# Kernel optimization log

Measured on AMD Instinct MI355X. Metric: run time of the kernel, lower is better.

Reference implementation:

```python
import jax, jax.numpy as jnp
import numpy as np

D_MODEL = 1024
N_HEADS = 16
HEAD_DIM = D_MODEL // N_HEADS
D_FF = 4096
B, S = 2, 2048


def layer_norm(x, gamma, beta, eps=1e-5):
    mu = jnp.mean(x, axis=-1, keepdims=True)
    var = jnp.mean(jnp.square(x - mu), axis=-1, keepdims=True)
    return (x - mu) * jax.lax.rsqrt(var + eps) * gamma + beta


def setup_inputs() -> dict:
    key = jax.random.key(0)
    ks = jax.random.split(key, 8)
    s = 0.02
    return {
        "x": jax.random.normal(ks[0], (B, S, D_MODEL), dtype=jnp.float32),
        "qkv_w": jax.random.normal(ks[1], (D_MODEL, 3 * D_MODEL), dtype=jnp.float32) * s,
        "qkv_b": jnp.zeros((3 * D_MODEL,), jnp.float32),
        "out_w": jax.random.normal(ks[2], (D_MODEL, D_MODEL), dtype=jnp.float32) * s,
        "out_b": jnp.zeros((D_MODEL,), jnp.float32),
        "attn_ln_g": jnp.ones((D_MODEL,), jnp.float32),
        "attn_ln_b": jnp.zeros((D_MODEL,), jnp.float32),
        "norm1_g": jnp.ones((D_MODEL,), jnp.float32),
        "norm1_b": jnp.zeros((D_MODEL,), jnp.float32),
        "ff_ln_g": jnp.ones((D_MODEL,), jnp.float32),
        "ff_ln_b": jnp.zeros((D_MODEL,), jnp.float32),
        "w1": jax.random.normal(ks[3], (D_MODEL, D_FF), dtype=jnp.float32) * s,
        "b1": jnp.zeros((D_FF,), jnp.float32),
        "w2": jax.random.normal(ks[4], (D_FF, D_MODEL), dtype=jnp.float32) * s,
        "b2": jnp.zeros((D_MODEL,), jnp.float32),
        "norm2_g": jnp.ones((D_MODEL,), jnp.float32),
        "norm2_b": jnp.zeros((D_MODEL,), jnp.float32),
    }


def reference(x, qkv_w, qkv_b, out_w, out_b, attn_ln_g, attn_ln_b,
              norm1_g, norm1_b, ff_ln_g, ff_ln_b, w1, b1, w2, b2,
              norm2_g, norm2_b):
    # --- MultiHeadAttention (pre-LN inside the attn block) ---
    h = layer_norm(x, attn_ln_g, attn_ln_b)
    qkv = h @ qkv_w + qkv_b                       # [B,S,3D]
    qkv = qkv.reshape(B, S, 3, N_HEADS, HEAD_DIM)
    q = jnp.transpose(qkv[:, :, 0], (0, 2, 1, 3))  # [B,H,S,hd]
    k = jnp.transpose(qkv[:, :, 1], (0, 2, 1, 3))
    v = jnp.transpose(qkv[:, :, 2], (0, 2, 1, 3))
    scale = HEAD_DIM ** -0.5
    scores = jnp.einsum("bhqd,bhkd->bhqk", q, k) * scale  # [B,H,S,S]
    attn = jax.nn.softmax(scores, axis=-1)
    ctx = jnp.einsum("bhqk,bhkd->bhqd", attn, v)
    ctx = jnp.transpose(ctx, (0, 2, 1, 3)).reshape(B, S, D_MODEL)
    attn_out = ctx @ out_w + out_b

    # residual + post-LN
    x = layer_norm(x + attn_out, norm1_g, norm1_b)

    # --- FeedForward (pre-LN inside the FF block, GELU) ---
    h = layer_norm(x, ff_ln_g, ff_ln_b)
    ff = jax.nn.gelu(h @ w1 + b1, approximate=False) @ w2 + b2

    # residual + post-LN
    return layer_norm(x + ff, norm2_g, norm2_b)
```

## Files before the change

kernel.cpp:

```cpp
#include <hip/hip_runtime.h>
#include <hip/hip_bf16.h>

typedef __attribute__((ext_vector_type(4))) float f32x4;
typedef __attribute__((ext_vector_type(16))) float f32x16;
typedef __attribute__((ext_vector_type(8))) short s16x8;
typedef __attribute__((ext_vector_type(4))) short s16x4;

#define DM 1024
#define NH 16
#define NB 2
#define NS 2048
#define NTOK (NB*NS)

__device__ __forceinline__ float b2f(short u){
  union { unsigned int i; float f; } c; c.i = ((unsigned int)(unsigned short)u) << 16; return c.f;
}
__device__ __forceinline__ short f2b(float f){
  __hip_bfloat16 h = __float2bfloat16(f);
  return __builtin_bit_cast(short, h);
}
__device__ __forceinline__ unsigned pk2(float lo, float hi){
  unsigned ul = __builtin_bit_cast(unsigned, lo);
  unsigned uh = __builtin_bit_cast(unsigned, hi);
  return (uh & 0xFFFF0000u) | (ul >> 16);
}
__device__ __forceinline__ float ex2(float x){
  float r;
  asm("v_exp_f32 %0, %1" : "=v"(r) : "v"(x));
  return r;
}
__device__ __forceinline__ void gload16(const void* g, void* l){
  __builtin_amdgcn_global_load_lds((const __attribute__((address_space(1))) void*)g,
                                   (__attribute__((address_space(3))) void*)l, 16, 0, 0);
}
__device__ __forceinline__ s16x4 tr16(const void* p){
  s16x4 r;
  asm volatile("ds_read_b64_tr_b16 %0, %1"
               : "=v"(r)
               : "v"((const __attribute__((address_space(3))) short*)p)
               : "memory");
  return r;
}

#define BARX { __builtin_amdgcn_sched_barrier(0); __builtin_amdgcn_s_barrier(); __builtin_amdgcn_sched_barrier(0); }
#define LGK  { asm volatile("s_waitcnt lgkmcnt(0)" ::: "memory"); __builtin_amdgcn_sched_barrier(0); }

template<int MIH>
__device__ __forceinline__ void rdA(s16x8 (&Af)[4][2], const short* Ab, int foff){
  #pragma unroll
  for (int m=0;m<4;m++)
    #pragma unroll
    for (int ks=0;ks<2;ks++)
      Af[m][ks] = *(const s16x8*)(Ab + (MIH*4+m)*1024 + ks*512 + foff);
}
template<int NIH>
__device__ __forceinline__ void rdB(s16x8 (&Bf)[4][2], const short* Bb, int foff){
  #pragma unroll
  for (int n=0;n<2;n++)
    #pragma unroll
    for (int ks=0;ks<2;ks++)
      Bf[NIH*2+n][ks] = *(const s16x8*)(Bb + (NIH*2+n)*1024 + ks*512 + foff);
}
template<int MIH,int NIH>
__device__ __forceinline__ void mmQ(f32x4 (&acc)[8][4], s16x8 (&Af)[4][2], s16x8 (&Bf)[4][2]){
  __builtin_amdgcn_s_setprio(1);
  #pragma unroll
  for (int m=0;m<4;m++)
    #pragma unroll
    for (int n=0;n<2;n++)
      #pragma unroll
      for (int ks=0;ks<2;ks++)
        acc[MIH*4+m][NIH*2+n] = __builtin_amdgcn_mfma_f32_16x16x32_bf16(
            Af[m][ks], Bf[NIH*2+n][ks], acc[MIH*4+m][NIH*2+n], 0,0,0);
  __builtin_amdgcn_s_setprio(0);
}

template<int GELU, int SPLITS>
__global__ __launch_bounds__(512,2) void gemm8p(
    const short* __restrict__ A, const short* __restrict__ Bt,
    const float* __restrict__ bias,
    short* __restrict__ C0, short* __restrict__ C1,
    short* __restrict__ C2, short* __restrict__ C3,
    int M, int N, int Ktot)
{
  __shared__ short Al[2*16384];
  __shared__ short Bl[2*16384];
  int tid = threadIdx.x, wid = tid>>6, lane = tid&63;
  int la = lane&15, lb = lane>>4;
  int z = blockIdx.z;
  const int Ksp = Ktot / SPLITS;
  short* C = (SPLITS==1) ? C0 : (z==0?C0 : z==1?C1 : z==2?C2 : C3);
  const short* Az  = A  + z*Ksp;
  const short* Btz = Bt + z*Ksp;
  int nbn = N>>8;
  int nwg = (M>>8)*nbn;
  int bid = (int)blockIdx.x;
  int sid = (bid&7)*(nwg>>3) + (bid>>3);
  int bm = sid / nbn, bn = sid % nbn;
  int wm2 = wid>>2, wn4 = wid&3;
  int bhalf = wn4>>1, bq4 = (wn4&1)*4;

  const short* aA0 = Az  + (size_t)(bm*256)*Ktot;
  const short* aA1 = Az  + (size_t)(bm*256+128)*Ktot;
  const short* bB0 = Btz + (size_t)(bn*256)*Ktot;
  const short* bB1 = Btz + (size_t)(bn*256+128)*Ktot;

  auto stG = [&](short* dstHalf, const short* srcRow0, int kt){
    #pragma unroll
    for (int c=0;c<2;c++){
      int s = c*8 + wid;
      int row = ((s>>1)<<4) + (lane>>2);
      int kk  = kt + ((s&1)<<5) + (((lane&3)<<3) ^ ((lane&32)>>1));
      gload16(srcRow0 + (size_t)row*Ktot + kk, dstHalf + s*512);
    }
  };

  int NJ = Ksp>>7;
  stG(&Al[0], aA0, 0);      stG(&Al[8192], aA1, 0);
  stG(&Bl[0], bB0, 0);      stG(&Bl[8192], bB1, 0);
  stG(&Bl[16384], bB0, 64); stG(&Bl[16384+8192], bB1, 64);
  asm volatile("s_waitcnt vmcnt(4)" ::: "memory");
  BARX;

  f32x4 acc[8][4] = {};
  s16x8 Af[4][2], Bf[4][2];
  int foff = la*32 + ((lb*8) ^ ((la&8)<<1));

  const short* Ab0c = &Al[wm2*8192];
  const short* Ab1c = &Al[16384 + wm2*8192];
  const short* Bb0c = &Bl[bhalf*8192 + bq4*1024];
  const short* Bb1c = &Bl[16384 + bhalf*8192 + bq4*1024];

  for (int j=0;j<NJ;j++){
    bool more = (j+1 < NJ);
    int ktA  = (2*j+1)*64;
    int ktN0 = (2*j+2)*64, ktN1 = (2*j+3)*64;
    rdA<0>(Af, Ab0c, foff); rdB<0>(Bf, Bb0c, foff);
    stG(&Al[16384], aA0, ktA);
    BARX; LGK; mmQ<0,0>(acc,Af,Bf); BARX;
    rdB<1>(Bf, Bb0c, foff);
    stG(&Al[16384+8192], aA1, ktA);
    BARX; LGK; mmQ<0,1>(acc,Af,Bf); BARX;
    rdA<1>(Af, Ab0c, foff);
    if (more) stG(&Bl[0], bB0, ktN0);
    BARX; LGK; mmQ<1,1>(acc,Af,Bf); BARX;
    if (more){ stG(&Bl[8192], bB1, ktN0);
               asm volatile("s_waitcnt vmcnt(4)" ::: "memory"); }
    else     { asm volatile("s_waitcnt vmcnt(0)" ::: "memory"); }
    BARX; mmQ<1,0>(acc,Af,Bf); BARX;
    rdA<0>(Af, Ab1c, foff); rdB<0>(Bf, Bb1c, foff);
    if (more) stG(&Al[0], aA0, ktN0);
    BARX; LGK; mmQ<0,0>(acc,Af,Bf); BARX;
    rdB<1>(Bf, Bb1c, foff);
    if (more) stG(&Al[8192], aA1, ktN0);
    BARX; LGK; mmQ<0,1>(acc,Af,Bf); BARX;
    rdA<1>(Af, Ab1c, foff);
    if (more) stG(&Bl[16384], bB0, ktN1);
    BARX; LGK; mmQ<1,1>(acc,Af,Bf); BARX;
    if (more){ stG(&Bl[16384+8192], bB1, ktN1);
               asm volatile("s_waitcnt vmcnt(4)" ::: "memory"); }
    else     { asm volatile("s_waitcnt vmcnt(0)" ::: "memory"); }
    BARX; mmQ<1,0>(acc,Af,Bf); BARX;
  }

  #pragma unroll
  for (int ni=0;ni<4;ni++){
    int col = bn*256 + wn4*64 + ni*16 + la;
    float bv = (SPLITS==1 || z==0) ? bias[col] : 0.0f;
    #pragma unroll
    for (int mi=0;mi<8;mi++){
      int row0 = bm*256 + wm2*128 + mi*16 + lb*4;
      #pragma unroll
      for (int j=0;j<4;j++){
        float v = acc[mi][ni][j] + bv;
        if (GELU) v = 0.5f*v*(1.0f + erff(v*0.70710678118f));
        C[(size_t)(row0+j)*N + col] = f2b(v);
      }
    }
  }
}

__global__ __launch_bounds__(512,1) void attn_fwd(const short* __restrict__ qkv, short* __restrict__ ctx)
{
  __shared__ short KlS[2*4096];
  __shared__ short VlS[2*4096];
  __shared__ float stats[8*32];
  char* Kl = (char*)KlS; char* Vl = (char*)VlS;
  int tid=threadIdx.x, w=tid>>6, lane=tid&63;
  int q5=lane&31, hi=lane>>5, la=lane&15, lb0=(lane>>4)&1;
  int qt=blockIdx.x, bh=blockIdx.y;
  int b=bh>>4, h=bh&15;
  int q0w = qt*256 + w*32;

  const float QSC = 0.125f * 1.44269504f;
  const short* qp = qkv + (size_t)(b*NS+q0w+q5)*3072 + h*64 + hi*8;
  s16x8 qf[4];
  #pragma unroll
  for (int ds=0; ds<4; ds++){
    s16x8 v = *(const s16x8*)(qp + ds*16);
    #pragma unroll
    for (int j=0;j<8;j++) v[j] = f2b(b2f(v[j])*QSC);
    qf[ds]=v;
  }

  int krow = 8*w + (lane>>3);
  int kcolS = (((lane&7) ^ ((lane>>3)&7)) << 3);
  const short* Ksrc = qkv + (size_t)(b*NS+krow)*3072 + h*64 + 1024 + kcolS;
  int vk = 16*(w&3) + 8*hi + 4*lb0 + ((lane>>1)&3);
  int vd = 32*(w>>2) + 16*((lane>>3)&1) + 8*(lane&1);
  const short* Vsrc = qkv + (size_t)(b*NS+vk)*3072 + h*64 + 2048 + vd;

  int sw = (q5&7)<<4;
  int baseK = q5*128 + ((hi<<4) ^ (sw&16)) + (sw&96);
  int baseV = hi*512 + lb0*128 + la*8;

  f32x16 cacc0={}, cacc1={};
  float mrow=-1e30f, lrow=0.f;
  const size_t tstep = (size_t)64*3072;

  gload16(Ksrc, Kl + w*1024);
  gload16(Vsrc, Vl + w*1024);
  __syncthreads();
  int cur=0;

  for (int t=0;t<NS/64;t++){
    if (t+1 < NS/64){
      gload16(Ksrc + (size_t)(t+1)*tstep, Kl + (cur^1)*8192 + w*1024);
      gload16(Vsrc + (size_t)(t+1)*tstep, Vl + (cur^1)*8192 + w*1024);
    }
    const char* Kb = Kl + cur*8192;
    f32x16 s0={}, s1={};
    #pragma unroll
    for (int ds=0; ds<4; ds++){
      s16x8 k0 = *(const s16x8*)(Kb + (baseK ^ (ds<<5)));
      s16x8 k1 = *(const s16x8*)(Kb + 4096 + (baseK ^ (ds<<5)));
      s0 = __builtin_amdgcn_mfma_f32_32x32x16_bf16(k0, qf[ds], s0, 0,0,0);
      s1 = __builtin_amdgcn_mfma_f32_32x32x16_bf16(k1, qf[ds], s1, 0,0,0);
    }
    float pmax = s0[0];
    #pragma unroll
    for (int r=1;r<16;r++) pmax = fmaxf(pmax, s0[r]);
    #pragma unroll
    for (int r=0;r<16;r++) pmax = fmaxf(pmax, s1[r]);
    pmax = fmaxf(pmax, __shfl_xor(pmax, 32, 64));
    if (__any(pmax > mrow + 8.f)){
      float mnew = fmaxf(mrow, pmax);
      float corr = ex2(mrow - mnew);
      if (!hi) stats[w*32+q5] = corr;
      LGK;
      lrow *= corr; mrow = mnew;
      #pragma unroll
      for (int r=0;r<16;r++){
        float c = stats[w*32 + ((r&3)+8*(r>>2)+4*hi)];
        cacc0[r]*=c; cacc1[r]*=c;
      }
    }
    float rs = 0.f;
    #pragma unroll
    for (int r=0;r<16;r++){ float p=ex2(s0[r]-mrow); s0[r]=p; rs+=p; }
    #pragma unroll
    for (int r=0;r<16;r++){ float p=ex2(s1[r]-mrow); s1[r]=p; rs+=p; }
    rs += __shfl_xor(rs, 32, 64);
    lrow += rs;
    unsigned int D0[4][2], D1[4][2], R0[4][2], R1[4][2];
    #pragma unroll
    for (int bb=0;bb<4;bb++)
      #pragma unroll
      for (int hh=0;hh<2;hh++){
        D0[bb][hh] = pk2(s0[4*bb+2*hh], s0[4*bb+2*hh+1]);
        D1[bb][hh] = pk2(s1[4*bb+2*hh], s1[4*bb+2*hh+1]);
      }
    #pragma unroll
    for (int bb=0;bb<4;bb++)
      #pragma unroll
      for (int hh=0;hh<2;hh++){
        R0[bb][hh] = (unsigned int)__shfl_xor((int)D0[bb][hh], 32, 64);
        R1[bb][hh] = (unsigned int)__shfl_xor((int)D1[bb][hh], 32, 64);
      }
    union PA { unsigned int u[4]; s16x8 v; } pa[4];
    #pragma unroll
    for (int e=0;e<2;e++)
      #pragma unroll
      for (int hh=0;hh<2;hh++){
        pa[e].u[hh]     = hi ? R0[2*e+1][hh] : D0[2*e][hh];
        pa[e].u[2+hh]   = hi ? D0[2*e+1][hh] : R0[2*e][hh];
        pa[2+e].u[hh]   = hi ? R1[2*e+1][hh] : D1[2*e][hh];
        pa[2+e].u[2+hh] = hi ? D1[2*e+1][hh] : R1[2*e][hh];
      }
    const char* Vb = Vl + cur*8192;
    #pragma unroll
    for (int ks=0;ks<4;ks++){
      s16x4 t00 = tr16(Vb + ks*1024 +        0 + baseV);
      s16x4 t01 = tr16(Vb + ks*1024 +      256 + baseV);
      s16x4 t10 = tr16(Vb + ks*1024 + 4096     + baseV);
      s16x4 t11 = tr16(Vb + ks*1024 + 4096+256 + baseV);
      LGK;
      union { s16x4 hh[2]; s16x8 v; } u0, u1;
      u0.hh[0]=t00; u0.hh[1]=t01;
      u1.hh[0]=t10; u1.hh[1]=t11;
      cacc0 = __builtin_amdgcn_mfma_f32_32x32x16_bf16(pa[ks].v, u0.v, cacc0, 0,0,0);
      cacc1 = __builtin_amdgcn_mfma_f32_32x32x16_bf16(pa[ks].v, u1.v, cacc1, 0,0,0);
    }
    __syncthreads();
    cur ^= 1;
  }
  if (!hi) stats[w*32+q5] = 1.0f/lrow;
  LGK;
  #pragma unroll
  for (int r=0;r<16;r++){
    int q = (r&3)+8*(r>>2)+4*hi;
    float linv = stats[w*32+q];
    size_t row = (size_t)(b*NS + q0w + q)*DM + h*64;
    ctx[row + q5]      = f2b(cacc0[r]*linv);
    ctx[row + 32 + q5] = f2b(cacc1[r]*linv);
  }
}

__device__ __forceinline__ void wred2(float& s, float& ss){
  #pragma unroll
  for (int m=1;m<64;m<<=1){ s += __shfl_xor(s,m,64); ss += __shfl_xor(ss,m,64); }
}

__global__ __launch_bounds__(256) void ln_in(const float* __restrict__ x,
    const float* __restrict__ g, const float* __restrict__ be, short* __restrict__ out)
{
  int row=blockIdx.x, tid=threadIdx.x;
  __shared__ float r1[4], r2[4];
  float4 v = ((const float4*)(x + (size_t)row*DM))[tid];
  float s=v.x+v.y+v.z+v.w, ss=v.x*v.x+v.y*v.y+v.z*v.z+v.w*v.w;
  wred2(s,ss);
  if ((tid&63)==0){ r1[tid>>6]=s; r2[tid>>6]=ss; }
  __syncthreads();
  s=r1[0]+r1[1]+r1[2]+r1[3]; ss=r2[0]+r2[1]+r2[2]+r2[3];
  float mu=s*(1.f/DM);
  float rstd=rsqrtf(ss*(1.f/DM)-mu*mu+1e-5f);
  float4 gv=((const float4*)g)[tid], bv=((const float4*)be)[tid];
  s16x4 o;
  o[0]=f2b((v.x-mu)*rstd*gv.x+bv.x);
  o[1]=f2b((v.y-mu)*rstd*gv.y+bv.y);
  o[2]=f2b((v.z-mu)*rstd*gv.z+bv.z);
  o[3]=f2b((v.w-mu)*rstd*gv.w+bv.w);
  *(s16x4*)(out + (size_t)row*DM + tid*4) = o;
}

__global__ __launch_bounds__(256) void ln_chain(const float* __restrict__ x,
    const short* __restrict__ p0, const short* __restrict__ p1,
    const short* __restrict__ p2, const short* __restrict__ p3,
    const float* __restrict__ g1, const float* __restrict__ be1,
    const float* __restrict__ g2, const float* __restrict__ be2,
    float* __restrict__ x1, short* __restrict__ h2)
{
  int row=blockIdx.x, tid=threadIdx.x;
  __shared__ float r1[4], r2[4], r3[4], r4[4];
  size_t off = (size_t)row*DM + tid*4;
  float4 xv = ((const float4*)(x + (size_t)row*DM))[tid];
  s16x4 a0=*(const s16x4*)(p0+off), a1=*(const s16x4*)(p1+off);
  s16x4 a2=*(const s16x4*)(p2+off), a3=*(const s16x4*)(p3+off);
  float4 y;
  y.x = xv.x + b2f(a0[0])+b2f(a1[0])+b2f(a2[0])+b2f(a3[0]);
  y.y = xv.y + b2f(a0[1])+b2f(a1[1])+b2f(a2[1])+b2f(a3[1]);
  y.z = xv.z + b2f(a0[2])+b2f(a1[2])+b2f(a2[2])+b2f(a3[2]);
  y.w = xv.w + b2f(a0[3])+b2f(a1[3])+b2f(a2[3])+b2f(a3[3]);
  float s=y.x+y.y+y.z+y.w, ss=y.x*y.x+y.y*y.y+y.z*y.z+y.w*y.w;
  wred2(s,ss);
  if ((tid&63)==0){ r1[tid>>6]=s; r2[tid>>6]=ss; }
  __syncthreads();
  s=r1[0]+r1[1]+r1[2]+r1[3]; ss=r2[0]+r2[1]+r2[2]+r2[3];
  float mu=s*(1.f/DM);
  float rstd=rsqrtf(ss*(1.f/DM)-mu*mu+1e-5f);
  float4 g1v=((const float4*)g1)[tid], b1v=((const float4*)be1)[tid];
  float4 xo;
  xo.x=(y.x-mu)*rstd*g1v.x+b1v.x;
  xo.y=(y.y-mu)*rstd*g1v.y+b1v.y;
  xo.z=(y.z-mu)*rstd*g1v.z+b1v.z;
  xo.w=(y.w-mu)*rstd*g1v.w+b1v.w;
  ((float4*)(x1 + (size_t)row*DM))[tid] = xo;
  float s2=xo.x+xo.y+xo.z+xo.w, ss2=xo.x*xo.x+xo.y*xo.y+xo.z*xo.z+xo.w*xo.w;
  wred2(s2,ss2);
  if ((tid&63)==0){ r3[tid>>6]=s2; r4[tid>>6]=ss2; }
  __syncthreads();
  s2=r3[0]+r3[1]+r3[2]+r3[3]; ss2=r4[0]+r4[1]+r4[2]+r4[3];
  float mu2=s2*(1.f/DM);
  float rstd2=rsqrtf(ss2*(1.f/DM)-mu2*mu2+1e-5f);
  float4 g2v=((const float4*)g2)[tid], b2v=((const float4*)be2)[tid];
  s16x4 o;
  o[0]=f2b((xo.x-mu2)*rstd2*g2v.x+b2v.x);
  o[1]=f2b((xo.y-mu2)*rstd2*g2v.y+b2v.y);
  o[2]=f2b((xo.z-mu2)*rstd2*g2v.z+b2v.z);
  o[3]=f2b((xo.w-mu2)*rstd2*g2v.w+b2v.w);
  *(s16x4*)(h2 + off) = o;
}

__global__ __launch_bounds__(256) void ln_out_k(const float* __restrict__ x1,
    const short* __restrict__ p0, const short* __restrict__ p1,
    const short* __restrict__ p2, const short* __restrict__ p3,
    const float* __restrict__ g, const float* __restrict__ be, float* __restrict__ out)
{
  int row=blockIdx.x, tid=threadIdx.x;
  __shared__ float r1[4], r2[4];
  size_t off = (size_t)row*DM + tid*4;
  float4 xv = ((const float4*)(x1 + (size_t)row*DM))[tid];
  s16x4 a0=*(const s16x4*)(p0+off), a1=*(const s16x4*)(p1+off);
  s16x4 a2=*(const s16x4*)(p2+off), a3=*(const s16x4*)(p3+off);
  float4 y;
  y.x = xv.x + b2f(a0[0])+b2f(a1[0])+b2f(a2[0])+b2f(a3[0]);
  y.y = xv.y + b2f(a0[1])+b2f(a1[1])+b2f(a2[1])+b2f(a3[1]);
  y.z = xv.z + b2f(a0[2])+b2f(a1[2])+b2f(a2[2])+b2f(a3[2]);
  y.w = xv.w + b2f(a0[3])+b2f(a1[3])+b2f(a2[3])+b2f(a3[3]);
  float s=y.x+y.y+y.z+y.w, ss=y.x*y.x+y.y*y.y+y.z*y.z+y.w*y.w;
  wred2(s,ss);
  if ((tid&63)==0){ r1[tid>>6]=s; r2[tid>>6]=ss; }
  __syncthreads();
  s=r1[0]+r1[1]+r1[2]+r1[3]; ss=r2[0]+r2[1]+r2[2]+r2[3];
  float mu=s*(1.f/DM);
  float rstd=rsqrtf(ss*(1.f/DM)-mu*mu+1e-5f);
  float4 gv=((const float4*)g)[tid], bv=((const float4*)be)[tid];
  float4 o;
  o.x=(y.x-mu)*rstd*gv.x+bv.x;
  o.y=(y.y-mu)*rstd*gv.y+bv.y;
  o.z=(y.z-mu)*rstd*gv.z+bv.z;
  o.w=(y.w-mu)*rstd*gv.w+bv.w;
  ((float4*)(out + (size_t)row*DM))[tid] = o;
}

__global__ __launch_bounds__(256) void cast_t(const float* __restrict__ w, short* __restrict__ wt, int R, int C)
{
  __shared__ short t[64][65];
  int nbr = R>>6;
  int br = (int)blockIdx.x % nbr, bc = (int)blockIdx.x / nbr;
  int tid = threadIdx.x;
  #pragma unroll
  for (int i=0;i<4;i++){
    int c = i*256 + tid;
    int r = c>>4, c4 = (c&15)*4;
    float4 v = *(const float4*)(w + (size_t)(br*64 + r)*C + bc*64 + c4);
    t[r][c4+0]=f2b(v.x); t[r][c4+1]=f2b(v.y); t[r][c4+2]=f2b(v.z); t[r][c4+3]=f2b(v.w);
  }
  __syncthreads();
  #pragma unroll
  for (int i=0;i<4;i++){
    int c = i*256 + tid;
    int oc = c>>4, c4 = (c&15)*4;
    s16x4 p;
    p[0]=t[c4+0][oc]; p[1]=t[c4+1][oc]; p[2]=t[c4+2][oc]; p[3]=t[c4+3][oc];
    *(s16x4*)&wt[(size_t)(bc*64 + oc)*R + br*64 + c4] = p;
  }
}

extern "C" void kernel_launch(void* const* d_in, const int* in_sizes, int n_in,
                              void* d_out, int out_size, void* d_ws, size_t ws_size,
                              hipStream_t stream)
{
  const float* x      = (const float*)d_in[0];
  const float* qkv_w  = (const float*)d_in[1];
  const float* qkv_b  = (const float*)d_in[2];
  const float* out_w  = (const float*)d_in[3];
  const float* out_b  = (const float*)d_in[4];
  const float* aln_g  = (const float*)d_in[5];
  const float* aln_b  = (const float*)d_in[6];
  const float* n1_g   = (const float*)d_in[7];
  const float* n1_b   = (const float*)d_in[8];
  const float* fln_g  = (const float*)d_in[9];
  const float* fln_b  = (const float*)d_in[10];
  const float* w1     = (const float*)d_in[11];
  const float* b1     = (const float*)d_in[12];
  const float* w2     = (const float*)d_in[13];
  const float* b2     = (const float*)d_in[14];
  const float* n2_g   = (const float*)d_in[15];
  const float* n2_b   = (const float*)d_in[16];

  char* ws = (char*)d_ws;
  short* w2T   = (short*)(ws + 0);
  short* w1T   = (short*)(ws + 8388608);
  short* woutT = (short*)(ws + 16777216);
  short* wqkvT = (short*)(ws + 18874368);
  short* h1    = (short*)(ws + 25165824);
  short* qkv   = (short*)(ws + 33554432);
  short* ctx   = (short*)(ws + 58720256);
  float* x1    = (float*)(ws + 67108864);
  short* ff1   = (short*)(ws + 33554432);
  short* Po0 = (short*)(ws + 25165824);
  short* Po1 = (short*)(ws + 33554432);
  short* Po2 = (short*)(ws + 41943040);
  short* Po3 = (short*)(ws + 50331648);
  short* Pf0 = (short*)(ws + 8388608);
  short* Pf1 = (short*)(ws + 16777216);
  short* Pf2 = (short*)(ws + 25165824);
  short* Pf3 = (short*)(ws + 83886080);
  float* outp  = (float*)d_out;

  cast_t<<<dim3(16*48),256,0,stream>>>(qkv_w, wqkvT, 1024, 3072);
  cast_t<<<dim3(16*16),256,0,stream>>>(out_w, woutT, 1024, 1024);
  cast_t<<<dim3(16*64),256,0,stream>>>(w1,    w1T,   1024, 4096);
  cast_t<<<dim3(64*16),256,0,stream>>>(w2,    w2T,   4096, 1024);

  ln_in<<<NTOK,256,0,stream>>>(x, aln_g, aln_b, h1);
  gemm8p<0,1><<<dim3(192,1,1),512,0,stream>>>(h1, wqkvT, qkv_b, qkv,qkv,qkv,qkv, 4096,3072,1024);
  attn_fwd<<<dim3(8,32),512,0,stream>>>(qkv, ctx);
  gemm8p<0,4><<<dim3(64,1,4),512,0,stream>>>(ctx, woutT, out_b, Po0,Po1,Po2,Po3, 4096,1024,1024);
  ln_chain<<<NTOK,256,0,stream>>>(x, Po0,Po1,Po2,Po3, n1_g,n1_b, fln_g,fln_b, x1, h1);
  gemm8p<1,1><<<dim3(256,1,1),512,0,stream>>>(h1, w1T, b1, ff1,ff1,ff1,ff1, 4096,4096,1024);
  gemm8p<0,4><<<dim3(64,1,4),512,0,stream>>>(ff1, w2T, b2, Pf0,Pf1,Pf2,Pf3, 4096,1024,4096);
  ln_out_k<<<NTOK,256,0,stream>>>(x1, Pf0,Pf1,Pf2,Pf3, n2_g,n2_b, outp);
}
```

Before: 273.0 us.

## Stage GEMM epilogue through LDS for coalesced stores and use tanh-GELU

The GEMM epilogue now writes bias-added results into shared memory and then copies full 256-column tile rows to global memory with 16-byte vector stores. Before, each lane did scattered 2-byte stores. The exact erf GELU is replaced by a tanh approximation computed with hardware exp2 and rcp instructions, which cuts transcendental cost in the FFN up-projection. This adds an extra barrier and LDS traffic, and the approximation changes numerics slightly relative to the exact GELU reference.

Result: faster. 260.3 us (-4.7%).

```diff
diff --git a/kernel.cpp b/kernel.cpp
--- a/kernel.cpp
+++ b/kernel.cpp
@@ -27,6 +27,11 @@
 __device__ __forceinline__ float ex2(float x){
   float r;
   asm("v_exp_f32 %0, %1" : "=v"(r) : "v"(x));
+  return r;
+}
+__device__ __forceinline__ float rcpf(float x){
+  float r;
+  asm("v_rcp_f32 %0, %1" : "=v"(r) : "v"(x));
   return r;
 }
 __device__ __forceinline__ void gload16(const void* g, void* l){
@@ -163,20 +168,38 @@
     BARX; mmQ<1,0>(acc,Af,Bf); BARX;
   }
 
+  short* halfC = wm2 ? Bl : Al;
   #pragma unroll
   for (int ni=0;ni<4;ni++){
-    int col = bn*256 + wn4*64 + ni*16 + la;
-    float bv = (SPLITS==1 || z==0) ? bias[col] : 0.0f;
+    int col = wn4*64 + ni*16 + la;
+    float bv = (SPLITS==1 || z==0) ? bias[bn*256 + col] : 0.0f;
     #pragma unroll
     for (int mi=0;mi<8;mi++){
-      int row0 = bm*256 + wm2*128 + mi*16 + lb*4;
+      int rloc = mi*16 + lb*4;
       #pragma unroll
       for (int j=0;j<4;j++){
         float v = acc[mi][ni][j] + bv;
-        if (GELU) v = 0.5f*v*(1.0f + erff(v*0.70710678118f));
-        C[(size_t)(row0+j)*N + col] = f2b(v);
+        if (GELU){
+          float xx = v;
+          float y = xx*(0.79788456f + 0.035677408f*xx*xx);
+          float p = ex2(2.88539008f*y);
+          v = xx - xx*rcpf(p + 1.0f);
+        }
+        halfC[(rloc+j)*256 + col] = f2b(v);
       }
     }
+  }
+  BARX;
+  #pragma unroll
+  for (int i=0;i<8;i++){
+    int row = i*32 + (tid>>4);
+    int colc = (tid&15)*16;
+    const short* src = (i<4) ? &Al[(row&127)*256 + colc] : &Bl[(row&127)*256 + colc];
+    s16x8 v0 = *(const s16x8*)src;
+    s16x8 v1 = *(const s16x8*)(src+8);
+    short* dst = &C[(size_t)(bm*256+row)*N + bn*256 + colc];
+    *(s16x8*)dst = v0;
+    *(s16x8*)(dst+8) = v1;
   }
 }
 
```
